# Performance work log

Measured on AMD Instinct MI355X. Metric: run time of the kernel, lower is better.

The kernel has to match this reference:

```python
import jax, jax.numpy as jnp
import numpy as np

REP_DIM = 256
ATT_DIM = 256
AGRU_DIM = 256
BATCH = 64
MAX_FACTS = 512


def setup_inputs() -> dict:
    key = jax.random.key(0)
    ks = jax.random.split(key, 16)

    def lin(k, out_d, in_d):
        return jax.random.normal(k, (out_d, in_d), dtype=jnp.float32) / np.sqrt(in_d)

    inp = {
        "queries": jax.random.normal(ks[0], (BATCH, 1, REP_DIM), dtype=jnp.float32),
        "facts": jax.random.normal(ks[1], (BATCH, MAX_FACTS, REP_DIM), dtype=jnp.float32),
        "num_facts": jax.random.randint(ks[2], (BATCH,), 1, MAX_FACTS + 1, dtype=jnp.int32),
        "m_old": jax.random.normal(ks[3], (BATCH, 1, REP_DIM), dtype=jnp.float32),
        # attention MLP
        "W1_w": lin(ks[4], ATT_DIM, 4 * REP_DIM),
        "W1_b": jnp.zeros((ATT_DIM,), jnp.float32),
        "W2_w": lin(ks[5], 1, ATT_DIM),
        "W2_b": jnp.zeros((1,), jnp.float32),
        # attention GRU cell
        "Wr_w": lin(ks[6], AGRU_DIM, REP_DIM),
        "Ur_w": lin(ks[7], AGRU_DIM, AGRU_DIM),
        "Ur_b": jnp.zeros((AGRU_DIM,), jnp.float32),
        "Wg_w": lin(ks[8], AGRU_DIM, REP_DIM),
        "Ug_w": lin(ks[9], AGRU_DIM, AGRU_DIM),
        "Ug_b": jnp.zeros((AGRU_DIM,), jnp.float32),
        # output transform
        "Wt_w": lin(ks[10], REP_DIM, 2 * REP_DIM + AGRU_DIM),
        "Wt_b": jnp.zeros((REP_DIM,), jnp.float32),
    }
    return inp


def _forward(queries, facts, num_facts, m_old,
             W1_w, W1_b, W2_w, W2_b,
             Wr_w, Ur_w, Ur_b, Wg_w, Ug_w, Ug_b,
             Wt_w, Wt_b):
    B, T, D = facts.shape

    # ---- attention scores ----
    q = queries  # (B,1,D) broadcasts
    m = m_old
    z = jnp.concatenate(
        [facts * q, facts * m, jnp.abs(facts - q), jnp.abs(facts - m)], axis=2
    )  # (B,T,4D)
    Z = jnp.tanh(jnp.einsum("btf,af->bta", z, W1_w) + W1_b)
    Z = jnp.einsum("bta,oa->bto", Z, W2_w) + W2_b  # (B,T,1)
    mask = (jnp.arange(T)[None, :] < num_facts[:, None])[..., None]  # (B,T,1)
    Z = jnp.where(mask, Z, -jnp.inf)
    g = jax.nn.softmax(Z, axis=1)  # (B,T,1)

    # ---- attention GRU (sequential scan over facts) ----
    h0 = m_old[:, 0]  # (B,A)

    def step(h, xs):
        fact, g_t = xs  # (B,D), (B,1)
        r = jax.nn.sigmoid(fact @ Wr_w.T + h @ Ur_w.T + Ur_b)
        h_t = jnp.tanh(fact @ Wg_w.T + r * (h @ Ug_w.T + Ug_b))
        h_new = g_t * h_t + (1.0 - g_t) * h
        return h_new, h_new

    xs = (jnp.swapaxes(facts, 0, 1), jnp.swapaxes(g, 0, 1))  # (T,B,D),(T,B,1)
    _, states = jax.lax.scan(step, h0, xs)  # (T,B,A)
    c = jnp.take_along_axis(
        states, (num_facts - 1)[None, :, None].astype(jnp.int32), axis=0
    )[0]  # (B,A)

    # ---- next memory ----
    cat = jnp.concatenate([m_old[:, 0], c, queries[:, 0]], axis=1)
    m_new = jax.nn.relu(cat @ Wt_w.T + Wt_b)
    return m_new[:, None, :]  # (B,1,D)


def reference(queries, facts, num_facts, m_old,
              W1_w, W1_b, W2_w, W2_b,
              Wr_w, Ur_w, Ur_b, Wg_w, Ug_w, Ug_b,
              Wt_w, Wt_b):
    return _forward(queries, facts, num_facts, m_old,
                    W1_w, W1_b, W2_w, W2_b,
                    Wr_w, Ur_w, Ur_b, Wg_w, Ug_w, Ug_b,
                    Wt_w, Wt_b)
```

## Files before the change

kernel.cpp:

```cpp
#include <hip/hip_runtime.h>
#include <hip/hip_fp16.h>
#include <stdint.h>

#define B 64
#define T 512
#define D 256

typedef _Float16 f16;
typedef __attribute__((ext_vector_type(8))) _Float16 f16x8;
typedef __attribute__((ext_vector_type(4))) _Float16 f16x4;
typedef __attribute__((ext_vector_type(2))) _Float16 f16x2;
typedef __attribute__((ext_vector_type(4))) float f32x4;
typedef __attribute__((ext_vector_type(4))) unsigned int u32x4;

static __device__ __forceinline__ float dot2f(f16x2 a, f16x2 b, float c) {
  return __builtin_amdgcn_fdot2(a, b, c, false);
}
static __device__ __forceinline__ f16x2 as_h2(unsigned int u) {
  return __builtin_bit_cast(f16x2, u);
}

__global__ void k_convert(const float* __restrict__ W1, const float* __restrict__ Wr,
                          const float* __restrict__ Wg,
                          f16* __restrict__ W1h, f16* __restrict__ Wrh, f16* __restrict__ Wgh)
{
  const int64_t n1 = 256 * 1024, n2 = 65536, n3 = 65536;
  int64_t stride = (int64_t)gridDim.x * blockDim.x;
  for (int64_t i = (int64_t)blockIdx.x * blockDim.x + threadIdx.x; i < n1 + n2 + n3; i += stride) {
    if (i < n1)           W1h[i] = (f16)W1[i];
    else if (i < n1 + n2) Wrh[i - n1] = (f16)Wr[i - n1];
    else                  Wgh[i - n1 - n2] = (f16)Wg[i - n1 - n2];
  }
}

__global__ __launch_bounds__(256, 2) void k_attn(
    const float* __restrict__ facts, const float* __restrict__ queries,
    const float* __restrict__ m_old, const f16* __restrict__ W1h,
    const float* __restrict__ W1_b, const float* __restrict__ W2_w,
    const float* __restrict__ W2_b, float* __restrict__ Zlog)
{
  const int b = blockIdx.y;
  const int t0 = blockIdx.x * 32;
  const int tid = threadIdx.x;
  const int lane = tid & 63;
  const int wave = tid >> 6;
  const int lr = lane & 15;
  const int lg = lane >> 4;

  __shared__ float q_s[D], m_s[D];
  __shared__ __align__(16) char zbuf[32 * 2048];
  __shared__ float part[4][32];

  q_s[tid] = queries[b * D + tid];
  m_s[tid] = m_old[b * D + tid];
  __syncthreads();

  for (int e = tid; e < 32 * 128; e += 256) {
    int t = e >> 7;
    int j2 = e & 127;
    int j = j2 * 2;
    const float2 f2 = *(const float2*)(facts + ((int64_t)(b * T) + t0 + t) * D + j);
    float q0 = q_s[j], q1 = q_s[j + 1], mm0 = m_s[j], mm1 = m_s[j + 1];
    f16x2 z0; z0[0] = (f16)(f2.x * q0);        z0[1] = (f16)(f2.y * q1);
    f16x2 z1; z1[0] = (f16)(f2.x * mm0);       z1[1] = (f16)(f2.y * mm1);
    f16x2 z2; z2[0] = (f16)fabsf(f2.x - q0);   z2[1] = (f16)fabsf(f2.y - q1);
    f16x2 z3; z3[0] = (f16)fabsf(f2.x - mm0);  z3[1] = (f16)fabsf(f2.y - mm1);
    int xr = (t & 7) << 4;
    int base = t * 2048;
    *(f16x2*)(zbuf + ((base + (0 * 128 + j2) * 4) ^ xr)) = z0;
    *(f16x2*)(zbuf + ((base + (1 * 128 + j2) * 4) ^ xr)) = z1;
    *(f16x2*)(zbuf + ((base + (2 * 128 + j2) * 4) ^ xr)) = z2;
    *(f16x2*)(zbuf + ((base + (3 * 128 + j2) * 4) ^ xr)) = z3;
  }
  __syncthreads();

  const int n0 = wave * 64;
  f32x4 acc[2][4];
  #pragma unroll
  for (int i = 0; i < 2; ++i)
    #pragma unroll
    for (int j = 0; j < 4; ++j) acc[i][j] = (f32x4){0.f, 0.f, 0.f, 0.f};

  #pragma unroll 2
  for (int ks = 0; ks < 32; ++ks) {
    f16x8 af[2];
    #pragma unroll
    for (int mt = 0; mt < 2; ++mt) {
      int row = mt * 16 + lr;
      int byte = (row * 2048 + ks * 64 + lg * 16) ^ ((row & 7) << 4);
      af[mt] = *(const f16x8*)(zbuf + byte);
    }
    #pragma unroll
    for (int nt = 0; nt < 4; ++nt) {
      int a = n0 + nt * 16 + lr;
      f16x8 bf = *(const f16x8*)(W1h + (int64_t)a * 1024 + ks * 32 + lg * 8);
      acc[0][nt] = __builtin_amdgcn_mfma_f32_16x16x32_f16(af[0], bf, acc[0][nt], 0, 0, 0);
      acc[1][nt] = __builtin_amdgcn_mfma_f32_16x16x32_f16(af[1], bf, acc[1][nt], 0, 0, 0);
    }
  }

  float pr[2][4] = {{0.f, 0.f, 0.f, 0.f}, {0.f, 0.f, 0.f, 0.f}};
  #pragma unroll
  for (int nt = 0; nt < 4; ++nt) {
    int a = n0 + nt * 16 + lr;
    float b1 = W1_b[a];
    float w2 = W2_w[a];
    #pragma unroll
    for (int mt = 0; mt < 2; ++mt)
      #pragma unroll
      for (int r = 0; r < 4; ++r)
        pr[mt][r] += tanhf(acc[mt][nt][r] + b1) * w2;
  }
  #pragma unroll
  for (int mt = 0; mt < 2; ++mt)
    #pragma unroll
    for (int r = 0; r < 4; ++r) {
      float v = pr[mt][r];
      v += __shfl_xor(v, 1, 64);
      v += __shfl_xor(v, 2, 64);
      v += __shfl_xor(v, 4, 64);
      v += __shfl_xor(v, 8, 64);
      pr[mt][r] = v;
    }
  if ((lane & 15) == 0) {
    #pragma unroll
    for (int mt = 0; mt < 2; ++mt)
      #pragma unroll
      for (int r = 0; r < 4; ++r)
        part[wave][mt * 16 + lg * 4 + r] = pr[mt][r];
  }
  __syncthreads();
  if (tid < 32)
    Zlog[b * T + t0 + tid] = part[0][tid] + part[1][tid] + part[2][tid] + part[3][tid] + W2_b[0];
}

__global__ __launch_bounds__(256, 2) void k_factproj(
    const float* __restrict__ facts, const f16* __restrict__ Wrh, const f16* __restrict__ Wgh,
    const float* __restrict__ Ur_b, f16* __restrict__ Frh, f16* __restrict__ Fgh)
{
  const int b = blockIdx.y;
  const int t0 = blockIdx.x * 64;
  const int tid = threadIdx.x;
  const int lane = tid & 63;
  const int wave = tid >> 6;
  const int lr = lane & 15;
  const int lg = lane >> 4;

  __shared__ __align__(16) char albuf[64 * 512];

  for (int c = tid; c < 64 * 32; c += 256) {
    int row = c >> 5;
    int kc = c & 31;
    const float* src = facts + ((int64_t)(b * T) + t0 + row) * D + kc * 8;
    float4 x0 = *(const float4*)src;
    float4 x1 = *(const float4*)(src + 4);
    f16x8 v;
    v[0] = (f16)x0.x; v[1] = (f16)x0.y; v[2] = (f16)x0.z; v[3] = (f16)x0.w;
    v[4] = (f16)x1.x; v[5] = (f16)x1.y; v[6] = (f16)x1.z; v[7] = (f16)x1.w;
    int byte = (row * 512 + kc * 16) ^ ((row & 7) << 4);
    *(f16x8*)(albuf + byte) = v;
  }
  __syncthreads();

  f32x4 accr[16], accg[16];
  #pragma unroll
  for (int i = 0; i < 16; ++i) { accr[i] = (f32x4){0.f,0.f,0.f,0.f}; accg[i] = (f32x4){0.f,0.f,0.f,0.f}; }

  const int arow = wave * 16 + lr;
  #pragma unroll 2
  for (int ks = 0; ks < 8; ++ks) {
    int byte = (arow * 512 + ks * 64 + lg * 16) ^ ((arow & 7) << 4);
    f16x8 af = *(const f16x8*)(albuf + byte);
    #pragma unroll
    for (int nt = 0; nt < 16; ++nt) {
      int a = nt * 16 + lr;
      f16x8 br = *(const f16x8*)(Wrh + a * 256 + ks * 32 + lg * 8);
      f16x8 bg = *(const f16x8*)(Wgh + a * 256 + ks * 32 + lg * 8);
      accr[nt] = __builtin_amdgcn_mfma_f32_16x16x32_f16(af, br, accr[nt], 0, 0, 0);
      accg[nt] = __builtin_amdgcn_mfma_f32_16x16x32_f16(af, bg, accg[nt], 0, 0, 0);
    }
  }

  #pragma unroll
  for (int nt = 0; nt < 16; ++nt) {
    int col = nt * 16 + lr;
    float urb = Ur_b[col];
    #pragma unroll
    for (int r = 0; r < 4; ++r) {
      int t = t0 + wave * 16 + lg * 4 + r;
      int64_t off = ((int64_t)(b * T) + t) * D + col;
      Frh[off] = (f16)(accr[nt][r] + urb);
      Fgh[off] = (f16)(accg[nt][r]);
    }
  }
}

__global__ __launch_bounds__(512) void k_scan_v5(
    const float* __restrict__ Zlog, const int* __restrict__ num_facts,
    const f16* __restrict__ Frh, const f16* __restrict__ Fgh,
    const float* __restrict__ Ur_w, const float* __restrict__ Ug_w,
    const float* __restrict__ Ug_b, const float* __restrict__ m_old,
    const float* __restrict__ queries, const float* __restrict__ Wt_w,
    const float* __restrict__ Wt_b, float* __restrict__ out)
{
  const int b = blockIdx.x;
  const int tid = threadIdx.x;
  const int l = tid & 63;
  const int w = tid >> 6;
  const int kg = l & 7;
  const int rg = w * 8 + (l >> 3);
  const int r0 = rg * 4;
  const int nf = num_facts[b];

  __shared__ __align__(16) char hbuf[2][640];
  __shared__ float g_lds[512];
  __shared__ float red[8];
  __shared__ __align__(16) float cat_s[768];

  {
    float z = Zlog[b * 512 + tid];
    float v = (tid < nf) ? z : -INFINITY;
    float mx = v;
    #pragma unroll
    for (int s = 1; s < 64; s <<= 1) mx = fmaxf(mx, __shfl_xor(mx, s, 64));
    if (l == 0) red[w] = mx;
    __syncthreads();
    mx = red[0];
    #pragma unroll
    for (int j = 1; j < 8; ++j) mx = fmaxf(mx, red[j]);
    float e = (tid < nf) ? __expf(v - mx) : 0.f;
    float sum = e;
    #pragma unroll
    for (int s = 1; s < 64; s <<= 1) sum += __shfl_xor(sum, s, 64);
    __syncthreads();
    if (l == 0) red[w] = sum;
    __syncthreads();
    sum = red[0] + red[1] + red[2] + red[3] + red[4] + red[5] + red[6] + red[7];
    g_lds[tid] = e / sum;
  }

  f16x2 wR[4][16], wG[4][16];
  #pragma unroll
  for (int j = 0; j < 4; ++j) {
    const float* ur = Ur_w + (int64_t)(r0 + j) * 256 + kg * 32;
    const float* ug = Ug_w + (int64_t)(r0 + j) * 256 + kg * 32;
    #pragma unroll
    for (int q = 0; q < 8; ++q) {
      float4 a = *(const float4*)(ur + q * 4);
      float4 c = *(const float4*)(ug + q * 4);
      f16x2 p0; p0[0] = (f16)a.x; p0[1] = (f16)a.y;
      f16x2 p1; p1[0] = (f16)a.z; p1[1] = (f16)a.w;
      f16x2 q0; q0[0] = (f16)c.x; q0[1] = (f16)c.y;
      f16x2 q1; q1[0] = (f16)c.z; q1[1] = (f16)c.w;
      wR[j][q * 2 + 0] = p0;
      wR[j][q * 2 + 1] = p1;
      wG[j][q * 2 + 0] = q0;
      wG[j][q * 2 + 1] = q1;
    }
  }

  float4 h0 = *(const float4*)(m_old + (int64_t)b * 256 + r0);
  float h[4] = {h0.x, h0.y, h0.z, h0.w};
  float4 ub4 = *(const float4*)(Ug_b + r0);

  const int haddr = (r0 >> 5) * 80 + (r0 & 31) * 2;
  if (kg == 0) {
    f16x4 p; p[0] = (f16)h[0]; p[1] = (f16)h[1]; p[2] = (f16)h[2]; p[3] = (f16)h[3];
    *(f16x4*)(&hbuf[0][haddr]) = p;
  }

  const f16* __restrict__ frp = Frh + (int64_t)(b * T) * D + r0;
  const f16* __restrict__ fgp = Fgh + (int64_t)(b * T) * D + r0;
  f16x4 frv = *(const f16x4*)frp;
  f16x4 fgv = *(const f16x4*)fgp;

  __syncthreads();

  for (int t = 0; t < nf; ++t) {
    const char* hb = hbuf[t & 1];
    u32x4 hv0 = *(const u32x4*)(hb + kg * 80);
    u32x4 hv1 = *(const u32x4*)(hb + kg * 80 + 16);
    u32x4 hv2 = *(const u32x4*)(hb + kg * 80 + 32);
    u32x4 hv3 = *(const u32x4*)(hb + kg * 80 + 48);

    f16x4 nfr = {}, nfg = {};
    if (t + 1 < nf) {
      nfr = *(const f16x4*)(frp + (int64_t)(t + 1) * D);
      nfg = *(const f16x4*)(fgp + (int64_t)(t + 1) * D);
    }
    float gt = g_lds[t];

    unsigned hu[16] = {hv0.x, hv0.y, hv0.z, hv0.w, hv1.x, hv1.y, hv1.z, hv1.w,
                       hv2.x, hv2.y, hv2.z, hv2.w, hv3.x, hv3.y, hv3.z, hv3.w};
    float aR[4] = {0.f, 0.f, 0.f, 0.f};
    float aG[4] = {0.f, 0.f, 0.f, 0.f};
    #pragma unroll
    for (int i2 = 0; i2 < 16; ++i2) {
      f16x2 hh = as_h2(hu[i2]);
      #pragma unroll
      for (int j = 0; j < 4; ++j) {
        aR[j] = dot2f(hh, wR[j][i2], aR[j]);
        aG[j] = dot2f(hh, wG[j][i2], aG[j]);
      }
    }
    #pragma unroll
    for (int s = 1; s < 8; s <<= 1) {
      #pragma unroll
      for (int j = 0; j < 4; ++j) {
        aR[j] += __shfl_xor(aR[j], s, 64);
        aG[j] += __shfl_xor(aG[j], s, 64);
      }
    }

    f16x4 hp;
    #pragma unroll
    for (int j = 0; j < 4; ++j) {
      float fr = (float)frv[j];
      float fg = (float)fgv[j];
      float rr = __builtin_amdgcn_rcpf(1.f + __expf(-(fr + aR[j])));
      float y  = fg + rr * (aG[j] + ub4[j == 0 ? 0 : j]);
      float ht = 1.f - 2.f * __builtin_amdgcn_rcpf(1.f + __expf(2.f * y));
      h[j] = h[j] + gt * (ht - h[j]);
      hp[j] = (f16)h[j];
    }
    if (kg == 0)
      *(f16x4*)(&hbuf[(t + 1) & 1][haddr]) = hp;

    frv = nfr;
    fgv = nfg;
    __syncthreads();
  }

  if (tid < 256) {
    cat_s[tid]       = m_old[(int64_t)b * 256 + tid];
    cat_s[512 + tid] = queries[(int64_t)b * 256 + tid];
  }
  if (kg == 0) {
    cat_s[256 + r0 + 0] = h[0];
    cat_s[256 + r0 + 1] = h[1];
    cat_s[256 + r0 + 2] = h[2];
    cat_s[256 + r0 + 3] = h[3];
  }
  __syncthreads();
  if (tid < 256) {
    const float* wrow = Wt_w + (int64_t)tid * 768;
    float acc = 0.f;
    #pragma unroll 8
    for (int k = 0; k < 768; k += 4) {
      float4 wv = *(const float4*)(wrow + k);
      float4 c4 = *(const float4*)(cat_s + k);
      acc += wv.x * c4.x + wv.y * c4.y + wv.z * c4.z + wv.w * c4.w;
    }
    out[(int64_t)b * 256 + tid] = fmaxf(acc + Wt_b[tid], 0.f);
  }
}

extern "C" void kernel_launch(void* const* d_in, const int* in_sizes, int n_in,
                              void* d_out, int out_size, void* d_ws, size_t ws_size,
                              hipStream_t stream)
{
  const float* queries   = (const float*)d_in[0];
  const float* facts     = (const float*)d_in[1];
  const int*   num_facts = (const int*)d_in[2];
  const float* m_old     = (const float*)d_in[3];
  const float* W1_w = (const float*)d_in[4];
  const float* W1_b = (const float*)d_in[5];
  const float* W2_w = (const float*)d_in[6];
  const float* W2_b = (const float*)d_in[7];
  const float* Wr_w = (const float*)d_in[8];
  const float* Ur_w = (const float*)d_in[9];
  const float* Ur_b = (const float*)d_in[10];
  const float* Wg_w = (const float*)d_in[11];
  const float* Ug_w = (const float*)d_in[12];
  const float* Ug_b = (const float*)d_in[13];
  const float* Wt_w = (const float*)d_in[14];
  const float* Wt_b = (const float*)d_in[15];
  float* out = (float*)d_out;

  char* p = (char*)d_ws;
  auto alloc = [&](size_t bytes) { char* r = p; p += (bytes + 255) & ~(size_t)255; return r; };
  f16*   W1h  = (f16*)alloc((size_t)256 * 1024 * 2);
  f16*   Wrh  = (f16*)alloc((size_t)65536 * 2);
  f16*   Wgh  = (f16*)alloc((size_t)65536 * 2);
  float* Zlog = (float*)alloc((size_t)B * T * 4);
  f16*   Frh  = (f16*)alloc((size_t)B * T * D * 2);
  f16*   Fgh  = (f16*)alloc((size_t)B * T * D * 2);

  k_convert<<<dim3(768), dim3(256), 0, stream>>>(W1_w, Wr_w, Wg_w, W1h, Wrh, Wgh);
  k_attn<<<dim3(16, 64), dim3(256), 0, stream>>>(facts, queries, m_old, W1h, W1_b, W2_w, W2_b, Zlog);
  k_factproj<<<dim3(8, 64), dim3(256), 0, stream>>>(facts, Wrh, Wgh, Ur_b, Frh, Fgh);
  k_scan_v5<<<dim3(64), dim3(512), 0, stream>>>(Zlog, num_facts, Frh, Fgh, Ur_w, Ug_w, Ug_b,
                                                m_old, queries, Wt_w, Wt_b, out);
}
```

Baseline: 883.7 us.

## Repartition GRU scan across 256 threads with half-row dot products

The sequential scan kernel moves from 512 threads (8-way K split, 4 rows per group) to 256 threads, where each thread owns 2 output rows and half of K (128 elements). The recurrent weights live in registers at 256 f16x2 per thread. The per-step reduction shrinks from a 3-level shuffle to a single xor-32 shuffle, and fewer waves take part in each barrier. This aims to cut per-step latency on the serial critical path, at the cost of heavy register pressure (single wave per SIMD) and longer per-thread dot chains.

```diff
diff --git a/kernel.cpp b/kernel.cpp
--- a/kernel.cpp
+++ b/kernel.cpp
@@ -195,7 +195,7 @@
   }
 }
 
-__global__ __launch_bounds__(512) void k_scan_v5(
+__global__ __launch_bounds__(256, 1) void k_scan_v6(
     const float* __restrict__ Zlog, const int* __restrict__ num_facts,
     const f16* __restrict__ Frh, const f16* __restrict__ Fgh,
     const float* __restrict__ Ur_w, const float* __restrict__ Ug_w,
@@ -205,144 +205,158 @@
 {
   const int b = blockIdx.x;
   const int tid = threadIdx.x;
-  const int l = tid & 63;
+  const int lane = tid & 63;
   const int w = tid >> 6;
-  const int kg = l & 7;
-  const int rg = w * 8 + (l >> 3);
-  const int r0 = rg * 4;
+  const int q = lane >> 5;
+  const int p = w * 32 + (lane & 31);
   const int nf = num_facts[b];
 
-  __shared__ __align__(16) char hbuf[2][640];
+  __shared__ __align__(16) char hbuf[2][544];
   __shared__ float g_lds[512];
-  __shared__ float red[8];
+  __shared__ float redM[4], redS[4];
   __shared__ __align__(16) float cat_s[768];
 
   {
-    float z = Zlog[b * 512 + tid];
-    float v = (tid < nf) ? z : -INFINITY;
-    float mx = v;
+    float z0 = Zlog[b * 512 + tid];
+    float z1 = Zlog[b * 512 + 256 + tid];
+    float v0 = (tid < nf) ? z0 : -INFINITY;
+    float v1 = (tid + 256 < nf) ? z1 : -INFINITY;
+    float mx = fmaxf(v0, v1);
     #pragma unroll
     for (int s = 1; s < 64; s <<= 1) mx = fmaxf(mx, __shfl_xor(mx, s, 64));
-    if (l == 0) red[w] = mx;
+    if (lane == 0) redM[w] = mx;
     __syncthreads();
-    mx = red[0];
-    #pragma unroll
-    for (int j = 1; j < 8; ++j) mx = fmaxf(mx, red[j]);
-    float e = (tid < nf) ? __expf(v - mx) : 0.f;
-    float sum = e;
+    mx = fmaxf(fmaxf(redM[0], redM[1]), fmaxf(redM[2], redM[3]));
+    float e0 = (tid < nf) ? __expf(v0 - mx) : 0.f;
+    float e1 = (tid + 256 < nf) ? __expf(v1 - mx) : 0.f;
+    float sum = e0 + e1;
     #pragma unroll
     for (int s = 1; s < 64; s <<= 1) sum += __shfl_xor(sum, s, 64);
+    if (lane == 0) redS[w] = sum;
     __syncthreads();
-    if (l == 0) red[w] = sum;
-    __syncthreads();
-    sum = red[0] + red[1] + red[2] + red[3] + red[4] + red[5] + red[6] + red[7];
-    g_lds[tid] = e / sum;
-  }
-
-  f16x2 wR[4][16], wG[4][16];
-  #pragma unroll
-  for (int j = 0; j < 4; ++j) {
-    const float* ur = Ur_w + (int64_t)(r0 + j) * 256 + kg * 32;
-    const float* ug = Ug_w + (int64_t)(r0 + j) * 256 + kg * 32;
-    #pragma unroll
-    for (int q = 0; q < 8; ++q) {
-      float4 a = *(const float4*)(ur + q * 4);
-      float4 c = *(const float4*)(ug + q * 4);
-      f16x2 p0; p0[0] = (f16)a.x; p0[1] = (f16)a.y;
-      f16x2 p1; p1[0] = (f16)a.z; p1[1] = (f16)a.w;
-      f16x2 q0; q0[0] = (f16)c.x; q0[1] = (f16)c.y;
-      f16x2 q1; q1[0] = (f16)c.z; q1[1] = (f16)c.w;
-      wR[j][q * 2 + 0] = p0;
-      wR[j][q * 2 + 1] = p1;
-      wG[j][q * 2 + 0] = q0;
-      wG[j][q * 2 + 1] = q1;
-    }
-  }
-
-  float4 h0 = *(const float4*)(m_old + (int64_t)b * 256 + r0);
-  float h[4] = {h0.x, h0.y, h0.z, h0.w};
-  float4 ub4 = *(const float4*)(Ug_b + r0);
-
-  const int haddr = (r0 >> 5) * 80 + (r0 & 31) * 2;
-  if (kg == 0) {
-    f16x4 p; p[0] = (f16)h[0]; p[1] = (f16)h[1]; p[2] = (f16)h[2]; p[3] = (f16)h[3];
-    *(f16x4*)(&hbuf[0][haddr]) = p;
-  }
-
-  const f16* __restrict__ frp = Frh + (int64_t)(b * T) * D + r0;
-  const f16* __restrict__ fgp = Fgh + (int64_t)(b * T) * D + r0;
-  f16x4 frv = *(const f16x4*)frp;
-  f16x4 fgv = *(const f16x4*)fgp;
+    float inv = 1.f / (redS[0] + redS[1] + redS[2] + redS[3]);
+    g_lds[tid] = e0 * inv;
+    g_lds[256 + tid] = e1 * inv;
+  }
+
+  f16x2 wR[2][64], wG[2][64];
+  #pragma unroll
+  for (int j = 0; j < 2; ++j) {
+    const float* ur = Ur_w + (int64_t)(2 * p + j) * 256 + q * 128;
+    const float* ug = Ug_w + (int64_t)(2 * p + j) * 256 + q * 128;
+    #pragma unroll
+    for (int c = 0; c < 32; ++c) {
+      float4 a = *(const float4*)(ur + c * 4);
+      float4 g4 = *(const float4*)(ug + c * 4);
+      f16x2 p0; p0[0] = (f16)a.x;  p0[1] = (f16)a.y;
+      f16x2 p1; p1[0] = (f16)a.z;  p1[1] = (f16)a.w;
+      f16x2 q0; q0[0] = (f16)g4.x; q0[1] = (f16)g4.y;
+      f16x2 q1; q1[0] = (f16)g4.z; q1[1] = (f16)g4.w;
+      wR[j][c * 2 + 0] = p0;
+      wR[j][c * 2 + 1] = p1;
+      wG[j][c * 2 + 0] = q0;
+      wG[j][c * 2 + 1] = q1;
+    }
+  }
+
+  float2 h2 = *(const float2*)(m_old + (int64_t)b * 256 + 2 * p);
+  float h0 = h2.x, h1 = h2.y;
+  float2 ub2 = *(const float2*)(Ug_b + 2 * p);
+
+  const int waddr = 4 * p + (p >= 64 ? 16 : 0);
+  if (q == 0) {
+    f16x2 hp; hp[0] = (f16)h0; hp[1] = (f16)h1;
+    *(f16x2*)(&hbuf[0][waddr]) = hp;
+  }
+
+  const f16* __restrict__ frp = Frh + (int64_t)(b * T) * D + 2 * p;
+  const f16* __restrict__ fgp = Fgh + (int64_t)(b * T) * D + 2 * p;
+  f16x2 frv = *(const f16x2*)frp;
+  f16x2 fgv = *(const f16x2*)fgp;
 
   __syncthreads();
 
   for (int t = 0; t < nf; ++t) {
-    const char* hb = hbuf[t & 1];
-    u32x4 hv0 = *(const u32x4*)(hb + kg * 80);
-    u32x4 hv1 = *(const u32x4*)(hb + kg * 80 + 16);
-    u32x4 hv2 = *(const u32x4*)(hb + kg * 80 + 32);
-    u32x4 hv3 = *(const u32x4*)(hb + kg * 80 + 48);
-
-    f16x4 nfr = {}, nfg = {};
+    const char* hb = hbuf[t & 1] + q * 272;
+    u32x4 hv[4];
+    #pragma unroll
+    for (int c = 0; c < 4; ++c) hv[c] = *(const u32x4*)(hb + c * 16);
+    u32x4 hw[4];
+    #pragma unroll
+    for (int c = 0; c < 4; ++c) hw[c] = *(const u32x4*)(hb + 64 + c * 16);
+    u32x4 hx[4];
+    #pragma unroll
+    for (int c = 0; c < 4; ++c) hx[c] = *(const u32x4*)(hb + 128 + c * 16);
+    u32x4 hy[4];
+    #pragma unroll
+    for (int c = 0; c < 4; ++c) hy[c] = *(const u32x4*)(hb + 192 + c * 16);
+
+    f16x2 nfr = {}, nfg = {};
     if (t + 1 < nf) {
-      nfr = *(const f16x4*)(frp + (int64_t)(t + 1) * D);
-      nfg = *(const f16x4*)(fgp + (int64_t)(t + 1) * D);
+      nfr = *(const f16x2*)(frp + (int64_t)(t + 1) * D);
+      nfg = *(const f16x2*)(fgp + (int64_t)(t + 1) * D);
     }
     float gt = g_lds[t];
 
-    unsigned hu[16] = {hv0.x, hv0.y, hv0.z, hv0.w, hv1.x, hv1.y, hv1.z, hv1.w,
-                       hv2.x, hv2.y, hv2.z, hv2.w, hv3.x, hv3.y, hv3.z, hv3.w};
-    float aR[4] = {0.f, 0.f, 0.f, 0.f};
-    float aG[4] = {0.f, 0.f, 0.f, 0.f};
-    #pragma unroll
-    for (int i2 = 0; i2 < 16; ++i2) {
-      f16x2 hh = as_h2(hu[i2]);
-      #pragma unroll
-      for (int j = 0; j < 4; ++j) {
-        aR[j] = dot2f(hh, wR[j][i2], aR[j]);
-        aG[j] = dot2f(hh, wG[j][i2], aG[j]);
-      }
-    }
-    #pragma unroll
-    for (int s = 1; s < 8; s <<= 1) {
-      #pragma unroll
-      for (int j = 0; j < 4; ++j) {
-        aR[j] += __shfl_xor(aR[j], s, 64);
-        aG[j] += __shfl_xor(aG[j], s, 64);
-      }
-    }
-
-    f16x4 hp;
-    #pragma unroll
-    for (int j = 0; j < 4; ++j) {
-      float fr = (float)frv[j];
-      float fg = (float)fgv[j];
-      float rr = __builtin_amdgcn_rcpf(1.f + __expf(-(fr + aR[j])));
-      float y  = fg + rr * (aG[j] + ub4[j == 0 ? 0 : j]);
-      float ht = 1.f - 2.f * __builtin_amdgcn_rcpf(1.f + __expf(2.f * y));
-      h[j] = h[j] + gt * (ht - h[j]);
-      hp[j] = (f16)h[j];
-    }
-    if (kg == 0)
-      *(f16x4*)(&hbuf[(t + 1) & 1][haddr]) = hp;
-
+    float aR0a = 0.f, aR0b = 0.f, aR1a = 0.f, aR1b = 0.f;
+    float aG0a = 0.f, aG0b = 0.f, aG1a = 0.f, aG1b = 0.f;
+    unsigned hu[64];
+    #pragma unroll
+    for (int c = 0; c < 4; ++c) {
+      hu[c * 4 + 0]  = hv[c].x; hu[c * 4 + 1]  = hv[c].y; hu[c * 4 + 2]  = hv[c].z; hu[c * 4 + 3]  = hv[c].w;
+      hu[16 + c * 4 + 0] = hw[c].x; hu[16 + c * 4 + 1] = hw[c].y; hu[16 + c * 4 + 2] = hw[c].z; hu[16 + c * 4 + 3] = hw[c].w;
+      hu[32 + c * 4 + 0] = hx[c].x; hu[32 + c * 4 + 1] = hx[c].y; hu[32 + c * 4 + 2] = hx[c].z; hu[32 + c * 4 + 3] = hx[c].w;
+      hu[48 + c * 4 + 0] = hy[c].x; hu[48 + c * 4 + 1] = hy[c].y; hu[48 + c * 4 + 2] = hy[c].z; hu[48 + c * 4 + 3] = hy[c].w;
+    }
+    #pragma unroll
+    for (int i2 = 0; i2 < 32; ++i2) {
+      f16x2 ha = as_h2(hu[i2 * 2]);
+      f16x2 hbv = as_h2(hu[i2 * 2 + 1]);
+      aR0a = dot2f(ha, wR[0][i2 * 2], aR0a);
+      aR0b = dot2f(hbv, wR[0][i2 * 2 + 1], aR0b);
+      aR1a = dot2f(ha, wR[1][i2 * 2], aR1a);
+      aR1b = dot2f(hbv, wR[1][i2 * 2 + 1], aR1b);
+      aG0a = dot2f(ha, wG[0][i2 * 2], aG0a);
+      aG0b = dot2f(hbv, wG[0][i2 * 2 + 1], aG0b);
+      aG1a = dot2f(ha, wG[1][i2 * 2], aG1a);
+      aG1b = dot2f(hbv, wG[1][i2 * 2 + 1], aG1b);
+    }
+    float aR0 = aR0a + aR0b, aR1 = aR1a + aR1b;
+    float aG0 = aG0a + aG0b, aG1 = aG1a + aG1b;
+    aR0 += __shfl_xor(aR0, 32, 64);
+    aR1 += __shfl_xor(aR1, 32, 64);
+    aG0 += __shfl_xor(aG0, 32, 64);
+    aG1 += __shfl_xor(aG1, 32, 64);
+
+    {
+      float fr0 = (float)frv[0], fr1 = (float)frv[1];
+      float fg0 = (float)fgv[0], fg1 = (float)fgv[1];
+      float rr0 = __builtin_amdgcn_rcpf(1.f + __expf(-(fr0 + aR0)));
+      float rr1 = __builtin_amdgcn_rcpf(1.f + __expf(-(fr1 + aR1)));
+      float y0 = fg0 + rr0 * (aG0 + ub2.x);
+      float y1 = fg1 + rr1 * (aG1 + ub2.y);
+      float ht0 = 1.f - 2.f * __builtin_amdgcn_rcpf(1.f + __expf(2.f * y0));
+      float ht1 = 1.f - 2.f * __builtin_amdgcn_rcpf(1.f + __expf(2.f * y1));
+      h0 = h0 + gt * (ht0 - h0);
+      h1 = h1 + gt * (ht1 - h1);
+    }
+    if (q == 0) {
+      f16x2 hp; hp[0] = (f16)h0; hp[1] = (f16)h1;
+      *(f16x2*)(&hbuf[(t + 1) & 1][waddr]) = hp;
+    }
     frv = nfr;
     fgv = nfg;
     __syncthreads();
   }
 
-  if (tid < 256) {
-    cat_s[tid]       = m_old[(int64_t)b * 256 + tid];
-    cat_s[512 + tid] = queries[(int64_t)b * 256 + tid];
-  }
-  if (kg == 0) {
-    cat_s[256 + r0 + 0] = h[0];
-    cat_s[256 + r0 + 1] = h[1];
-    cat_s[256 + r0 + 2] = h[2];
-    cat_s[256 + r0 + 3] = h[3];
-  }
-  __syncthreads();
-  if (tid < 256) {
+  cat_s[tid]       = m_old[(int64_t)b * 256 + tid];
+  cat_s[512 + tid] = queries[(int64_t)b * 256 + tid];
+  if (q == 0) {
+    cat_s[256 + 2 * p]     = h0;
+    cat_s[256 + 2 * p + 1] = h1;
+  }
+  __syncthreads();
+  {
     const float* wrow = Wt_w + (int64_t)tid * 768;
     float acc = 0.f;
     #pragma unroll 8
@@ -389,6 +403,6 @@
   k_convert<<<dim3(768), dim3(256), 0, stream>>>(W1_w, Wr_w, Wg_w, W1h, Wrh, Wgh);
   k_attn<<<dim3(16, 64), dim3(256), 0, stream>>>(facts, queries, m_old, W1h, W1_b, W2_w, W2_b, Zlog);
   k_factproj<<<dim3(8, 64), dim3(256), 0, stream>>>(facts, Wrh, Wgh, Ur_b, Frh, Fgh);
-  k_scan_v5<<<dim3(64), dim3(512), 0, stream>>>(Zlog, num_facts, Frh, Fgh, Ur_w, Ug_w, Ug_b,
+  k_scan_v6<<<dim3(64), dim3(256), 0, stream>>>(Zlog, num_facts, Frh, Fgh, Ur_w, Ug_w, Ug_b,
                                                 m_old, queries, Wt_w, Wt_b, out);
 }
```

Measured after the change: 811.1 us. 1.09x faster.
